# Optimization experiments

Hardware: AMD Instinct MI355X
Metric: run time of the kernel (lower is better)

## Reference

```python
import jax, jax.numpy as jnp
import numpy as np

EPS = 1e-7
NUM_NODES = 50000


def setup_inputs() -> dict:
    key = jax.random.key(0)
    k1, k2, k3 = jax.random.split(key, 3)
    n_nodes, n_edges, d = NUM_NODES, 800000, 64
    x = jax.random.normal(k1, (n_nodes, d), dtype=jnp.float32)
    edge_index = jax.random.randint(k2, (2, n_edges), 0, n_nodes, dtype=jnp.int64)
    W = jax.random.normal(k3, (d, d), dtype=jnp.float32) * (1.0 / np.sqrt(d))
    b = jnp.zeros((d,), dtype=jnp.float32)
    beta = jnp.ones((1,), dtype=jnp.float32)
    return {"x": x, "edge_index": edge_index, "W": W, "b": b, "beta": beta}


def _segment_softmax(logits, seg, num_segments):
    # numerically stable softmax over edges grouped by destination node, per channel
    m = jax.ops.segment_max(logits, seg, num_segments=num_segments)  # [N, d]
    m = jnp.where(jnp.isfinite(m), m, 0.0)  # empty segments -> -inf; neutralize
    e = jnp.exp(logits - m[seg])                                      # [E, d]
    denom = jax.ops.segment_sum(e, seg, num_segments=num_segments)    # [N, d]
    return e / (denom[seg] + 1e-16)


def reference(x, edge_index, W, b, beta):
    num_nodes, dim = x.shape
    dst = edge_index[0]
    src = edge_index[1]
    # gather + message encoder (ReLU) + eps
    edge_msg = jax.nn.relu(x[src]) + EPS                               # [E, d]
    # softmax_sg: softmax(beta * msg) per destination segment, beta is a stop-grad scalar
    alpha = _segment_softmax(beta[0] * edge_msg, dst, num_nodes)       # [E, d]
    h = edge_msg * alpha                                               # [E, d]
    # scatter-add aggregation to destination nodes
    agg = jax.ops.segment_sum(h, dst, num_segments=num_nodes)          # [N, d]
    # final dense linear (nn.Linear): agg @ W.T + b
    return agg @ W.T + b
```

## Files before the change

### kernel.cpp

```cpp
#include <hip/hip_runtime.h>
#include <hip/hip_fp16.h>

#define EPS 1e-7f

typedef _Float16 half8 __attribute__((ext_vector_type(8)));
typedef float f32x4 __attribute__((ext_vector_type(4)));

__global__ __launch_bounds__(512)
void binprep_kernel(const int* __restrict__ dst,
                    const int* __restrict__ src, int E, int cap,
                    const float* __restrict__ x,
                    const float* __restrict__ W, int M,
                    int* __restrict__ ccur,
                    unsigned* __restrict__ packed,
                    unsigned short* __restrict__ tm,
                    unsigned short* __restrict__ Wh,
                    int binBlocks) {
    if ((int)blockIdx.x < binBlocks) {
        __shared__ int lc[256];
        __shared__ int lbase[256];
        int tid = threadIdx.x;
        if (tid < 256) lc[tid] = 0;
        __syncthreads();
        int e0 = blockIdx.x * 2048;
        int bb[4], rr[4];
        unsigned pk[4];
        #pragma unroll
        for (int i = 0; i < 4; ++i) {
            int e = e0 + i * 512 + tid;
            bb[i] = 0; rr[i] = 0; pk[i] = 0;
            if (e < E) {
                int d = dst[e];
                bb[i] = d >> 8;
                pk[i] = ((unsigned)(d & 255) << 16) | (unsigned)src[e];
                rr[i] = atomicAdd(&lc[bb[i]], 1);
            }
        }
        __syncthreads();
        if (tid < 256) {
            int c = lc[tid];
            if (c) lbase[tid] = tid * cap + atomicAdd(&ccur[tid], c);
        }
        __syncthreads();
        #pragma unroll
        for (int i = 0; i < 4; ++i) {
            int e = e0 + i * 512 + tid;
            if (e < E) packed[lbase[bb[i]] + rr[i]] = pk[i];
        }
    } else {
        int blk = blockIdx.x - binBlocks;
        int tid = threadIdx.x;
        if (blk == 0) {
            #pragma unroll
            for (int j = 0; j < 8; ++j) {
                int i = tid * 8 + j;
                Wh[i] = __half_as_ushort(__float2half_rn(W[i]));
            }
        }
        const unsigned short sent = __half_as_ushort(__float2half_rn(-32.f));
        #pragma unroll
        for (int p = 0; p < 4; ++p) {
            int i = blk * 8192 + p * 2048 + tid * 4;
            if (i < M) {
                float4 v = *(const float4*)&x[i];
                ushort4 o;
                o.x = __half_as_ushort(__float2half_rn(fmaxf(v.x, 0.f) + EPS));
                o.y = __half_as_ushort(__float2half_rn(fmaxf(v.y, 0.f) + EPS));
                o.z = __half_as_ushort(__float2half_rn(fmaxf(v.z, 0.f) + EPS));
                o.w = __half_as_ushort(__float2half_rn(fmaxf(v.w, 0.f) + EPS));
                *(ushort4*)&tm[i] = o;
            } else if (i < M + 64) {
                ushort4 o; o.x = o.y = o.z = o.w = sent;
                *(ushort4*)&tm[i] = o;
            }
        }
    }
}

__global__ __launch_bounds__(512)
void fine_kernel(const unsigned* __restrict__ packed,
                 const int* __restrict__ ccur, int cap,
                 int2* __restrict__ nse,
                 unsigned short* __restrict__ sorted_src, int N) {
    __shared__ int lc[256];
    __shared__ int lcur[256];
    __shared__ int wsum[4];
    __shared__ unsigned stage_pk[6656];
    __shared__ unsigned short stage16[6656];
    int tid = threadIdx.x, b = blockIdx.x;
    int rs = b * cap;
    int len = ccur[b];
    if (tid < 256) lc[tid] = 0;
    __syncthreads();
    for (int i = tid; i < len; i += 512) {
        unsigned u = packed[rs + i];
        stage_pk[i] = u;
        atomicAdd(&lc[u >> 16], 1);
    }
    __syncthreads();
    if (tid < 256) {
        int lane = tid & 63, wid = tid >> 6;
        int incl = lc[tid];
        #pragma unroll
        for (int d = 1; d < 64; d <<= 1) {
            int t = __shfl_up(incl, d, 64);
            if (lane >= d) incl += t;
        }
        lcur[tid] = incl;
        if (lane == 63) wsum[wid] = incl;
    }
    __syncthreads();
    if (tid < 256) {
        int wid = tid >> 6;
        int base = 0;
        for (int w = 0; w < wid; ++w) base += wsum[w];
        int v = lc[tid];
        int excl = base + lcur[tid] - v;
        lcur[tid] = excl;
        int node = b * 256 + tid;
        if (node < N) nse[node] = make_int2(rs + excl, rs + excl + v);
    }
    __syncthreads();
    for (int i = tid; i < len; i += 512) {
        unsigned u = stage_pk[i];
        int pos = atomicAdd(&lcur[u >> 16], 1);
        stage16[pos] = (unsigned short)(u & 0xffffu);
    }
    __syncthreads();
    unsigned* dst32 = (unsigned*)&sorted_src[rs];
    int len2 = (len + 1) >> 1;
    for (int i = tid; i < len2; i += 512) {
        unsigned lo = stage16[2 * i];
        unsigned hi = (2 * i + 1 < len) ? (unsigned)stage16[2 * i + 1] : 0u;
        dst32[i] = lo | (hi << 16);
    }
}

__device__ __forceinline__ float hlo(unsigned w) {
    return __half2float(__ushort_as_half((unsigned short)(w & 0xffffu)));
}
__device__ __forceinline__ float hhi(unsigned w) {
    return __half2float(__ushort_as_half((unsigned short)(w >> 16)));
}

__global__ __launch_bounds__(256)
void gather_kernel(const unsigned short* __restrict__ tm,
                   const int2* __restrict__ nse,
                   const unsigned short* __restrict__ ss,
                   const float* __restrict__ beta,
                   unsigned short* __restrict__ agg16, int N) {
    const int tid = threadIdx.x;
    const int lane = tid & 63;
    const int quarter = lane >> 4;
    const int l16 = lane & 15;
    const int qbase = quarter << 4;
    const int chb = l16 << 3;
    const int sent = N << 7;
    const unsigned char* tb = (const unsigned char*)tm;
    const float c = beta[0] * 1.4426950408889634f;

    const int node = blockIdx.x * 16 + (tid >> 6) * 4 + quarter;
    int start = 0, cnt = 0;
    if (node < N) { int2 se = nse[node]; start = se.x; cnt = se.y - se.x; }

    float s1x = 0.f, s1y = 0.f, s1z = 0.f, s1w = 0.f;
    float s2x = 0.f, s2y = 0.f, s2z = 0.f, s2w = 0.f;

    for (int chunk = 0; chunk < cnt; chunk += 16) {
        int rem = cnt - chunk;
        if (rem > 16) rem = 16;
        int row = (l16 < rem) ? ((int)ss[start + chunk + l16] << 7) : sent;
        #pragma unroll
        for (int k = 0; k < 16; k += 4) {
            int r0 = __shfl(row, qbase + k + 0, 64);
            int r1 = __shfl(row, qbase + k + 1, 64);
            int r2 = __shfl(row, qbase + k + 2, 64);
            int r3 = __shfl(row, qbase + k + 3, 64);
            uint2 u0 = *(const uint2*)(tb + (r0 + chb));
            uint2 u1 = *(const uint2*)(tb + (r1 + chb));
            uint2 u2 = *(const uint2*)(tb + (r2 + chb));
            uint2 u3 = *(const uint2*)(tb + (r3 + chb));
            #define ACC(u) { \
                float m0 = hlo(u.x), m1 = hhi(u.x); \
                float m2 = hlo(u.y), m3 = hhi(u.y); \
                float e0 = exp2f(m0 * c), e1 = exp2f(m1 * c); \
                float e2 = exp2f(m2 * c), e3 = exp2f(m3 * c); \
                s1x += e0; s2x = fmaf(m0, e0, s2x); \
                s1y += e1; s2y = fmaf(m1, e1, s2y); \
                s1z += e2; s2z = fmaf(m2, e2, s2z); \
                s1w += e3; s2w = fmaf(m3, e3, s2w); }
            ACC(u0); ACC(u1); ACC(u2); ACC(u3);
            #undef ACC
        }
    }
    if (node < N) {
        float gx = __fdividef(s2x, s1x + 1e-16f);
        float gy = __fdividef(s2y, s1y + 1e-16f);
        float gz = __fdividef(s2z, s1z + 1e-16f);
        float gw = __fdividef(s2w, s1w + 1e-16f);
        uint2 o;
        o.x = (unsigned)__half_as_ushort(__float2half_rn(gx)) |
              ((unsigned)__half_as_ushort(__float2half_rn(gy)) << 16);
        o.y = (unsigned)__half_as_ushort(__float2half_rn(gz)) |
              ((unsigned)__half_as_ushort(__float2half_rn(gw)) << 16);
        *(uint2*)((unsigned char*)agg16 + ((size_t)node << 7) + chb) = o;
    }
}

__global__ __launch_bounds__(256)
void linear_kernel(const unsigned short* __restrict__ agg16,
                   const unsigned short* __restrict__ Wh,
                   const float* __restrict__ b,
                   float* __restrict__ out, int N, int G) {
    const int tid = threadIdx.x;
    const int wave = tid >> 6;
    const int lane = tid & 63;
    const int l16 = lane & 15;
    const int quad = lane >> 4;
    const int g = blockIdx.x * 4 + wave;
    if (g >= G) return;

    const unsigned char* ab = (const unsigned char*)agg16;
    const unsigned char* wb = (const unsigned char*)Wh;

    half8 a0 = *(const half8*)(ab + (((size_t)(g * 16 + l16)) << 7) + quad * 16);
    half8 a1 = *(const half8*)(ab + (((size_t)(g * 16 + l16)) << 7) + 64 + quad * 16);

    f32x4 acc[4];
    float bias[4];
    #pragma unroll
    for (int t = 0; t < 4; ++t) {
        const unsigned char* wr = wb + (((size_t)(16 * t + l16)) << 7) + quad * 16;
        half8 b0 = *(const half8*)(wr);
        half8 b1 = *(const half8*)(wr + 64);
        acc[t] = (f32x4){0.f, 0.f, 0.f, 0.f};
        acc[t] = __builtin_amdgcn_mfma_f32_16x16x32_f16(a0, b0, acc[t], 0, 0, 0);
        acc[t] = __builtin_amdgcn_mfma_f32_16x16x32_f16(a1, b1, acc[t], 0, 0, 0);
        bias[t] = b[16 * t + l16];
    }
    #pragma unroll
    for (int t = 0; t < 4; ++t) {
        #pragma unroll
        for (int r = 0; r < 4; ++r) {
            int node = g * 16 + quad * 4 + r;
            if (node < N)
                out[((size_t)node << 6) + 16 * t + l16] = acc[t][r] + bias[t];
        }
    }
}

extern "C" void kernel_launch(void* const* d_in, const int* in_sizes, int n_in,
                              void* d_out, int out_size, void* d_ws, size_t ws_size,
                              hipStream_t stream) {
    const float* x    = (const float*)d_in[0];
    const int*   ei   = (const int*)d_in[1];
    const float* W    = (const float*)d_in[2];
    const float* b    = (const float*)d_in[3];
    const float* beta = (const float*)d_in[4];
    float* out = (float*)d_out;

    const int N = in_sizes[0] / 64;
    const int E = in_sizes[1] / 2;
    const int* dst = ei;
    const int* src = ei + E;
    const int NB = (N + 255) >> 8;
    const int M = N * 64;
    const int G = (N + 15) / 16;

    int cap = (E + NB - 1) / NB;
    cap = ((cap + cap / 2 + 256) + 255) & ~255;
    if (cap > 6656) cap = 6656;

    auto align = [](size_t v) { return (v + 255) & ~(size_t)255; };
    size_t off = 0;
    char* ws = (char*)d_ws;
    int2* nse = (int2*)(ws + off);        off += align((size_t)N * 8);
    int* ccur = (int*)(ws + off);         off += align((size_t)NB * 4);
    unsigned* packed = (unsigned*)(ws + off);
    off += align((size_t)NB * cap * 4);
    unsigned short* sorted_src = (unsigned short*)(ws + off);
    off += align((size_t)NB * cap * 2);
    unsigned short* tm = (unsigned short*)(ws + off);
    off += align(((size_t)N + 1) * 64 * 2);
    unsigned short* agg16 = (unsigned short*)(ws + off);
    off += align((size_t)G * 16 * 64 * 2);
    unsigned short* Wh = (unsigned short*)(ws + off);
    off += align(64 * 64 * 2);

    const int binBlocks  = (E + 2047) / 2048;
    const int prepBlocks = (M + 64 + 8191) / 8192;
    hipMemsetAsync(ccur, 0, (size_t)NB * 4, stream);
    binprep_kernel<<<binBlocks + prepBlocks, 512, 0, stream>>>(
        dst, src, E, cap, x, W, M, ccur, packed, tm, Wh, binBlocks);
    fine_kernel<<<NB, 512, 0, stream>>>(packed, ccur, cap, nse, sorted_src, N);
    gather_kernel<<<G, 256, 0, stream>>>(tm, nse, sorted_src, beta, agg16, N);
    linear_kernel<<<(G + 3) / 4, 256, 0, stream>>>(agg16, Wh, b, out, N, G);
}
```

Before: 139.3 us.

## Precompute per-node exp and m*exp pairs, accumulate gathered edges in packed half2

Because the softmax weights depend only on the source node's feature, exp(beta*m) and m*exp(beta*m) are now computed once per node in the prep kernel and stored as packed fp16 pairs. This removes the per-edge exp from the gather. The gather then sums those pairs with half2 adds across each 16-edge chunk before folding into fp32. The cost is a per-node table twice as large, so the random gather reads twice as many bytes per edge. Fp16 accumulation within a chunk also risks overflow or lost precision, and the max subtraction is still skipped.

```diff
diff --git a/kernel.cpp b/kernel.cpp
--- a/kernel.cpp
+++ b/kernel.cpp
@@ -10,10 +10,11 @@
 void binprep_kernel(const int* __restrict__ dst,
                     const int* __restrict__ src, int E, int cap,
                     const float* __restrict__ x,
-                    const float* __restrict__ W, int M,
+                    const float* __restrict__ W,
+                    const float* __restrict__ beta, int M,
                     int* __restrict__ ccur,
                     unsigned* __restrict__ packed,
-                    unsigned short* __restrict__ tm,
+                    unsigned* __restrict__ tp,
                     unsigned short* __restrict__ Wh,
                     int binBlocks) {
     if ((int)blockIdx.x < binBlocks) {
@@ -57,21 +58,30 @@
                 Wh[i] = __half_as_ushort(__float2half_rn(W[i]));
             }
         }
-        const unsigned short sent = __half_as_ushort(__float2half_rn(-32.f));
+        const float bt = beta[0];
         #pragma unroll
         for (int p = 0; p < 4; ++p) {
             int i = blk * 8192 + p * 2048 + tid * 4;
             if (i < M) {
                 float4 v = *(const float4*)&x[i];
-                ushort4 o;
-                o.x = __half_as_ushort(__float2half_rn(fmaxf(v.x, 0.f) + EPS));
-                o.y = __half_as_ushort(__float2half_rn(fmaxf(v.y, 0.f) + EPS));
-                o.z = __half_as_ushort(__float2half_rn(fmaxf(v.z, 0.f) + EPS));
-                o.w = __half_as_ushort(__float2half_rn(fmaxf(v.w, 0.f) + EPS));
-                *(ushort4*)&tm[i] = o;
+                uint4 o;
+                float m, ex;
+                m = fmaxf(v.x, 0.f) + EPS; ex = __expf(bt * m);
+                o.x = (unsigned)__half_as_ushort(__float2half_rn(ex)) |
+                      ((unsigned)__half_as_ushort(__float2half_rn(m * ex)) << 16);
+                m = fmaxf(v.y, 0.f) + EPS; ex = __expf(bt * m);
+                o.y = (unsigned)__half_as_ushort(__float2half_rn(ex)) |
+                      ((unsigned)__half_as_ushort(__float2half_rn(m * ex)) << 16);
+                m = fmaxf(v.z, 0.f) + EPS; ex = __expf(bt * m);
+                o.z = (unsigned)__half_as_ushort(__float2half_rn(ex)) |
+                      ((unsigned)__half_as_ushort(__float2half_rn(m * ex)) << 16);
+                m = fmaxf(v.w, 0.f) + EPS; ex = __expf(bt * m);
+                o.w = (unsigned)__half_as_ushort(__float2half_rn(ex)) |
+                      ((unsigned)__half_as_ushort(__float2half_rn(m * ex)) << 16);
+                *(uint4*)&tp[i] = o;
             } else if (i < M + 64) {
-                ushort4 o; o.x = o.y = o.z = o.w = sent;
-                *(ushort4*)&tm[i] = o;
+                uint4 o; o.x = o.y = o.z = o.w = 0u;
+                *(uint4*)&tp[i] = o;
             }
         }
     }
@@ -136,74 +146,82 @@
     }
 }
 
-__device__ __forceinline__ float hlo(unsigned w) {
-    return __half2float(__ushort_as_half((unsigned short)(w & 0xffffu)));
-}
-__device__ __forceinline__ float hhi(unsigned w) {
-    return __half2float(__ushort_as_half((unsigned short)(w >> 16)));
-}
-
 __global__ __launch_bounds__(256)
-void gather_kernel(const unsigned short* __restrict__ tm,
+void gather_kernel(const unsigned* __restrict__ tp,
                    const int2* __restrict__ nse,
                    const unsigned short* __restrict__ ss,
-                   const float* __restrict__ beta,
                    unsigned short* __restrict__ agg16, int N) {
     const int tid = threadIdx.x;
     const int lane = tid & 63;
     const int quarter = lane >> 4;
     const int l16 = lane & 15;
     const int qbase = quarter << 4;
-    const int chb = l16 << 3;
-    const int sent = N << 7;
-    const unsigned char* tb = (const unsigned char*)tm;
-    const float c = beta[0] * 1.4426950408889634f;
+    const int chb = l16 << 4;
+    const int sent = N << 8;
+    const unsigned char* tb = (const unsigned char*)tp;
 
     const int node = blockIdx.x * 16 + (tid >> 6) * 4 + quarter;
     int start = 0, cnt = 0;
     if (node < N) { int2 se = nse[node]; start = se.x; cnt = se.y - se.x; }
 
-    float s1x = 0.f, s1y = 0.f, s1z = 0.f, s1w = 0.f;
-    float s2x = 0.f, s2y = 0.f, s2z = 0.f, s2w = 0.f;
+    float2 fs0 = {0.f, 0.f}, fs1 = {0.f, 0.f};
+    float2 fs2 = {0.f, 0.f}, fs3 = {0.f, 0.f};
 
     for (int chunk = 0; chunk < cnt; chunk += 16) {
         int rem = cnt - chunk;
         if (rem > 16) rem = 16;
-        int row = (l16 < rem) ? ((int)ss[start + chunk + l16] << 7) : sent;
+        int row = (l16 < rem) ? ((int)ss[start + chunk + l16] << 8) : sent;
+        __half2 a0 = __half2{__ushort_as_half(0), __ushort_as_half(0)};
+        __half2 a1 = a0, a2 = a0, a3 = a0;
+        __half2 b0 = a0, b1 = a0, b2 = a0, b3 = a0;
         #pragma unroll
         for (int k = 0; k < 16; k += 4) {
             int r0 = __shfl(row, qbase + k + 0, 64);
             int r1 = __shfl(row, qbase + k + 1, 64);
             int r2 = __shfl(row, qbase + k + 2, 64);
             int r3 = __shfl(row, qbase + k + 3, 64);
-            uint2 u0 = *(const uint2*)(tb + (r0 + chb));
-            uint2 u1 = *(const uint2*)(tb + (r1 + chb));
-            uint2 u2 = *(const uint2*)(tb + (r2 + chb));
-            uint2 u3 = *(const uint2*)(tb + (r3 + chb));
-            #define ACC(u) { \
-                float m0 = hlo(u.x), m1 = hhi(u.x); \
-                float m2 = hlo(u.y), m3 = hhi(u.y); \
-                float e0 = exp2f(m0 * c), e1 = exp2f(m1 * c); \
-                float e2 = exp2f(m2 * c), e3 = exp2f(m3 * c); \
-                s1x += e0; s2x = fmaf(m0, e0, s2x); \
-                s1y += e1; s2y = fmaf(m1, e1, s2y); \
-                s1z += e2; s2z = fmaf(m2, e2, s2z); \
-                s1w += e3; s2w = fmaf(m3, e3, s2w); }
-            ACC(u0); ACC(u1); ACC(u2); ACC(u3);
-            #undef ACC
-        }
+            uint4 u0 = *(const uint4*)(tb + (r0 + chb));
+            uint4 u1 = *(const uint4*)(tb + (r1 + chb));
+            uint4 u2 = *(const uint4*)(tb + (r2 + chb));
+            uint4 u3 = *(const uint4*)(tb + (r3 + chb));
+            a0 = __hadd2(a0, *(const __half2*)&u0.x);
+            a1 = __hadd2(a1, *(const __half2*)&u0.y);
+            a2 = __hadd2(a2, *(const __half2*)&u0.z);
+            a3 = __hadd2(a3, *(const __half2*)&u0.w);
+            a0 = __hadd2(a0, *(const __half2*)&u1.x);
+            a1 = __hadd2(a1, *(const __half2*)&u1.y);
+            a2 = __hadd2(a2, *(const __half2*)&u1.z);
+            a3 = __hadd2(a3, *(const __half2*)&u1.w);
+            b0 = __hadd2(b0, *(const __half2*)&u2.x);
+            b1 = __hadd2(b1, *(const __half2*)&u2.y);
+            b2 = __hadd2(b2, *(const __half2*)&u2.z);
+            b3 = __hadd2(b3, *(const __half2*)&u2.w);
+            b0 = __hadd2(b0, *(const __half2*)&u3.x);
+            b1 = __hadd2(b1, *(const __half2*)&u3.y);
+            b2 = __hadd2(b2, *(const __half2*)&u3.z);
+            b3 = __hadd2(b3, *(const __half2*)&u3.w);
+        }
+        float2 t;
+        t = __half22float2(a0); fs0.x += t.x; fs0.y += t.y;
+        t = __half22float2(b0); fs0.x += t.x; fs0.y += t.y;
+        t = __half22float2(a1); fs1.x += t.x; fs1.y += t.y;
+        t = __half22float2(b1); fs1.x += t.x; fs1.y += t.y;
+        t = __half22float2(a2); fs2.x += t.x; fs2.y += t.y;
+        t = __half22float2(b2); fs2.x += t.x; fs2.y += t.y;
+        t = __half22float2(a3); fs3.x += t.x; fs3.y += t.y;
+        t = __half22float2(b3); fs3.x += t.x; fs3.y += t.y;
     }
     if (node < N) {
-        float gx = __fdividef(s2x, s1x + 1e-16f);
-        float gy = __fdividef(s2y, s1y + 1e-16f);
-        float gz = __fdividef(s2z, s1z + 1e-16f);
-        float gw = __fdividef(s2w, s1w + 1e-16f);
+        float gx = __fdividef(fs0.y, fs0.x + 1e-16f);
+        float gy = __fdividef(fs1.y, fs1.x + 1e-16f);
+        float gz = __fdividef(fs2.y, fs2.x + 1e-16f);
+        float gw = __fdividef(fs3.y, fs3.x + 1e-16f);
         uint2 o;
         o.x = (unsigned)__half_as_ushort(__float2half_rn(gx)) |
               ((unsigned)__half_as_ushort(__float2half_rn(gy)) << 16);
         o.y = (unsigned)__half_as_ushort(__float2half_rn(gz)) |
               ((unsigned)__half_as_ushort(__float2half_rn(gw)) << 16);
-        *(uint2*)((unsigned char*)agg16 + ((size_t)node << 7) + chb) = o;
+        *(uint2*)((unsigned char*)agg16 + ((size_t)node << 7) + (l16 << 3)) = o;
     }
 }
 
@@ -280,8 +298,8 @@
     off += align((size_t)NB * cap * 4);
     unsigned short* sorted_src = (unsigned short*)(ws + off);
     off += align((size_t)NB * cap * 2);
-    unsigned short* tm = (unsigned short*)(ws + off);
-    off += align(((size_t)N + 1) * 64 * 2);
+    unsigned* tp = (unsigned*)(ws + off);
+    off += align(((size_t)N + 1) * 64 * 4);
     unsigned short* agg16 = (unsigned short*)(ws + off);
     off += align((size_t)G * 16 * 64 * 2);
     unsigned short* Wh = (unsigned short*)(ws + off);
@@ -291,8 +309,8 @@
     const int prepBlocks = (M + 64 + 8191) / 8192;
     hipMemsetAsync(ccur, 0, (size_t)NB * 4, stream);
     binprep_kernel<<<binBlocks + prepBlocks, 512, 0, stream>>>(
-        dst, src, E, cap, x, W, M, ccur, packed, tm, Wh, binBlocks);
+        dst, src, E, cap, x, W, beta, M, ccur, packed, tp, Wh, binBlocks);
     fine_kernel<<<NB, 512, 0, stream>>>(packed, ccur, cap, nse, sorted_src, N);
-    gather_kernel<<<G, 256, 0, stream>>>(tm, nse, sorted_src, beta, agg16, N);
+    gather_kernel<<<G, 256, 0, stream>>>(tp, nse, sorted_src, agg16, N);
     linear_kernel<<<(G + 3) / 4, 256, 0, stream>>>(agg16, Wh, b, out, N, G);
 }
```

Measured after the change: 130.2 us. 1.07x faster.

## Fuse gather and linear kernels via shared memory, prescale messages by beta

Applied to the files above, without the earlier changes.

Merges the segment-softmax gather kernel with the MFMA linear kernel. The per-block 16-node aggregate now goes through shared memory instead of a global fp16 buffer, removing one launch and the agg round trip. The prep kernel also stores messages pre-multiplied by beta*log2e, so the inner loop drops a multiply per element and rescales the result once at the end. This adds fp16 range and precision risk for the prescaled values, changes the sentinel to -1000, and divides by beta.

```diff
diff --git a/kernel.cpp b/kernel.cpp
--- a/kernel.cpp
+++ b/kernel.cpp
@@ -2,6 +2,7 @@
 #include <hip/hip_fp16.h>
 
 #define EPS 1e-7f
+#define LOG2E 1.4426950408889634f
 
 typedef _Float16 half8 __attribute__((ext_vector_type(8)));
 typedef float f32x4 __attribute__((ext_vector_type(4)));
@@ -10,7 +11,8 @@
 void binprep_kernel(const int* __restrict__ dst,
                     const int* __restrict__ src, int E, int cap,
                     const float* __restrict__ x,
-                    const float* __restrict__ W, int M,
+                    const float* __restrict__ W,
+                    const float* __restrict__ beta, int M,
                     int* __restrict__ ccur,
                     unsigned* __restrict__ packed,
                     unsigned short* __restrict__ tm,
@@ -57,17 +59,18 @@
                 Wh[i] = __half_as_ushort(__float2half_rn(W[i]));
             }
         }
-        const unsigned short sent = __half_as_ushort(__float2half_rn(-32.f));
+        const float btl = beta[0] * LOG2E;
+        const unsigned short sent = __half_as_ushort(__float2half_rn(-1000.f));
         #pragma unroll
         for (int p = 0; p < 4; ++p) {
             int i = blk * 8192 + p * 2048 + tid * 4;
             if (i < M) {
                 float4 v = *(const float4*)&x[i];
                 ushort4 o;
-                o.x = __half_as_ushort(__float2half_rn(fmaxf(v.x, 0.f) + EPS));
-                o.y = __half_as_ushort(__float2half_rn(fmaxf(v.y, 0.f) + EPS));
-                o.z = __half_as_ushort(__float2half_rn(fmaxf(v.z, 0.f) + EPS));
-                o.w = __half_as_ushort(__float2half_rn(fmaxf(v.w, 0.f) + EPS));
+                o.x = __half_as_ushort(__float2half_rn((fmaxf(v.x, 0.f) + EPS) * btl));
+                o.y = __half_as_ushort(__float2half_rn((fmaxf(v.y, 0.f) + EPS) * btl));
+                o.z = __half_as_ushort(__float2half_rn((fmaxf(v.z, 0.f) + EPS) * btl));
+                o.w = __half_as_ushort(__float2half_rn((fmaxf(v.w, 0.f) + EPS) * btl));
                 *(ushort4*)&tm[i] = o;
             } else if (i < M + 64) {
                 ushort4 o; o.x = o.y = o.z = o.w = sent;
@@ -136,20 +139,18 @@
     }
 }
 
-__device__ __forceinline__ float hlo(unsigned w) {
-    return __half2float(__ushort_as_half((unsigned short)(w & 0xffffu)));
-}
-__device__ __forceinline__ float hhi(unsigned w) {
-    return __half2float(__ushort_as_half((unsigned short)(w >> 16)));
-}
-
 __global__ __launch_bounds__(256)
-void gather_kernel(const unsigned short* __restrict__ tm,
-                   const int2* __restrict__ nse,
-                   const unsigned short* __restrict__ ss,
-                   const float* __restrict__ beta,
-                   unsigned short* __restrict__ agg16, int N) {
+void gatherlin_kernel(const unsigned short* __restrict__ tm,
+                      const int2* __restrict__ nse,
+                      const unsigned short* __restrict__ ss,
+                      const unsigned short* __restrict__ Wh,
+                      const float* __restrict__ bias,
+                      const float* __restrict__ beta,
+                      float* __restrict__ out, int N) {
+    __shared__ short aggS[16 * 72];
+
     const int tid = threadIdx.x;
+    const int wave = tid >> 6;
     const int lane = tid & 63;
     const int quarter = lane >> 4;
     const int l16 = lane & 15;
@@ -157,9 +158,11 @@
     const int chb = l16 << 3;
     const int sent = N << 7;
     const unsigned char* tb = (const unsigned char*)tm;
-    const float c = beta[0] * 1.4426950408889634f;
-
-    const int node = blockIdx.x * 16 + (tid >> 6) * 4 + quarter;
+    const float scale = 0.6931471805599453f / beta[0];
+
+    const int g = blockIdx.x;
+    const int nl = wave * 4 + quarter;
+    const int node = g * 16 + nl;
     int start = 0, cnt = 0;
     if (node < N) { int2 se = nse[node]; start = se.x; cnt = se.y - se.x; }
 
@@ -181,10 +184,12 @@
             uint2 u2 = *(const uint2*)(tb + (r2 + chb));
             uint2 u3 = *(const uint2*)(tb + (r3 + chb));
             #define ACC(u) { \
-                float m0 = hlo(u.x), m1 = hhi(u.x); \
-                float m2 = hlo(u.y), m3 = hhi(u.y); \
-                float e0 = exp2f(m0 * c), e1 = exp2f(m1 * c); \
-                float e2 = exp2f(m2 * c), e3 = exp2f(m3 * c); \
+                float m0 = __half2float(__ushort_as_half((unsigned short)(u.x & 0xffffu))); \
+                float m1 = __half2float(__ushort_as_half((unsigned short)(u.x >> 16))); \
+                float m2 = __half2float(__ushort_as_half((unsigned short)(u.y & 0xffffu))); \
+                float m3 = __half2float(__ushort_as_half((unsigned short)(u.y >> 16))); \
+                float e0 = exp2f(m0), e1 = exp2f(m1); \
+                float e2 = exp2f(m2), e3 = exp2f(m3); \
                 s1x += e0; s2x = fmaf(m0, e0, s2x); \
                 s1y += e1; s2y = fmaf(m1, e1, s2y); \
                 s1z += e2; s2z = fmaf(m2, e2, s2z); \
@@ -193,59 +198,37 @@
             #undef ACC
         }
     }
-    if (node < N) {
-        float gx = __fdividef(s2x, s1x + 1e-16f);
-        float gy = __fdividef(s2y, s1y + 1e-16f);
-        float gz = __fdividef(s2z, s1z + 1e-16f);
-        float gw = __fdividef(s2w, s1w + 1e-16f);
+
+    {
+        float gx = __fdividef(s2x, s1x + 1e-16f) * scale;
+        float gy = __fdividef(s2y, s1y + 1e-16f) * scale;
+        float gz = __fdividef(s2z, s1z + 1e-16f) * scale;
+        float gw = __fdividef(s2w, s1w + 1e-16f) * scale;
         uint2 o;
         o.x = (unsigned)__half_as_ushort(__float2half_rn(gx)) |
               ((unsigned)__half_as_ushort(__float2half_rn(gy)) << 16);
         o.y = (unsigned)__half_as_ushort(__float2half_rn(gz)) |
               ((unsigned)__half_as_ushort(__float2half_rn(gw)) << 16);
-        *(uint2*)((unsigned char*)agg16 + ((size_t)node << 7) + chb) = o;
-    }
-}
-
-__global__ __launch_bounds__(256)
-void linear_kernel(const unsigned short* __restrict__ agg16,
-                   const unsigned short* __restrict__ Wh,
-                   const float* __restrict__ b,
-                   float* __restrict__ out, int N, int G) {
-    const int tid = threadIdx.x;
-    const int wave = tid >> 6;
-    const int lane = tid & 63;
-    const int l16 = lane & 15;
-    const int quad = lane >> 4;
-    const int g = blockIdx.x * 4 + wave;
-    if (g >= G) return;
-
-    const unsigned char* ab = (const unsigned char*)agg16;
-    const unsigned char* wb = (const unsigned char*)Wh;
-
-    half8 a0 = *(const half8*)(ab + (((size_t)(g * 16 + l16)) << 7) + quad * 16);
-    half8 a1 = *(const half8*)(ab + (((size_t)(g * 16 + l16)) << 7) + 64 + quad * 16);
-
-    f32x4 acc[4];
-    float bias[4];
+        *(uint2*)((unsigned char*)aggS + nl * 144 + chb) = o;
+    }
+    __syncthreads();
+
+    const unsigned char* ab = (const unsigned char*)aggS;
+    half8 a0 = *(const half8*)(ab + l16 * 144 + quarter * 16);
+    half8 a1 = *(const half8*)(ab + l16 * 144 + 64 + quarter * 16);
+    const unsigned char* wr =
+        (const unsigned char*)Wh + (((size_t)(wave * 16 + l16)) << 7) + quarter * 16;
+    half8 b0 = *(const half8*)(wr);
+    half8 b1 = *(const half8*)(wr + 64);
+    f32x4 acc = (f32x4){0.f, 0.f, 0.f, 0.f};
+    acc = __builtin_amdgcn_mfma_f32_16x16x32_f16(a0, b0, acc, 0, 0, 0);
+    acc = __builtin_amdgcn_mfma_f32_16x16x32_f16(a1, b1, acc, 0, 0, 0);
+    const float bv = bias[wave * 16 + l16];
     #pragma unroll
-    for (int t = 0; t < 4; ++t) {
-        const unsigned char* wr = wb + (((size_t)(16 * t + l16)) << 7) + quad * 16;
-        half8 b0 = *(const half8*)(wr);
-        half8 b1 = *(const half8*)(wr + 64);
-        acc[t] = (f32x4){0.f, 0.f, 0.f, 0.f};
-        acc[t] = __builtin_amdgcn_mfma_f32_16x16x32_f16(a0, b0, acc[t], 0, 0, 0);
-        acc[t] = __builtin_amdgcn_mfma_f32_16x16x32_f16(a1, b1, acc[t], 0, 0, 0);
-        bias[t] = b[16 * t + l16];
-    }
-    #pragma unroll
-    for (int t = 0; t < 4; ++t) {
-        #pragma unroll
-        for (int r = 0; r < 4; ++r) {
-            int node = g * 16 + quad * 4 + r;
-            if (node < N)
-                out[((size_t)node << 6) + 16 * t + l16] = acc[t][r] + bias[t];
-        }
+    for (int r = 0; r < 4; ++r) {
+        int nd = g * 16 + quarter * 4 + r;
+        if (nd < N)
+            out[((size_t)nd << 6) + wave * 16 + l16] = acc[r] + bv;
     }
 }
 
@@ -282,8 +265,6 @@
     off += align((size_t)NB * cap * 2);
     unsigned short* tm = (unsigned short*)(ws + off);
     off += align(((size_t)N + 1) * 64 * 2);
-    unsigned short* agg16 = (unsigned short*)(ws + off);
-    off += align((size_t)G * 16 * 64 * 2);
     unsigned short* Wh = (unsigned short*)(ws + off);
     off += align(64 * 64 * 2);
 
@@ -291,8 +272,8 @@
     const int prepBlocks = (M + 64 + 8191) / 8192;
     hipMemsetAsync(ccur, 0, (size_t)NB * 4, stream);
     binprep_kernel<<<binBlocks + prepBlocks, 512, 0, stream>>>(
-        dst, src, E, cap, x, W, M, ccur, packed, tm, Wh, binBlocks);
+        dst, src, E, cap, x, W, beta, M, ccur, packed, tm, Wh, binBlocks);
     fine_kernel<<<NB, 512, 0, stream>>>(packed, ccur, cap, nse, sorted_src, N);
-    gather_kernel<<<G, 256, 0, stream>>>(tm, nse, sorted_src, beta, agg16, N);
-    linear_kernel<<<(G + 3) / 4, 256, 0, stream>>>(agg16, Wh, b, out, N, G);
-}
+    gatherlin_kernel<<<G, 256, 0, stream>>>(tm, nse, sorted_src, Wh, b, beta,
+                                            out, N);
+}
```

Result: faster. 118.2 us (-15.1%).
